# Kernel optimization log

Measured on AMD Instinct MI355X. Metric: run time of the kernel, lower is better.

Reference implementation:

```python
import jax, jax.numpy as jnp
import numpy as np
from jax import lax

B, T, F = 8, 512, 128          # batch, mel time, mel freq
DM, DS, DC, EXP, NL = 384, 16, 4, 2, 12
DI = EXP * DM                   # 768 inner width
DTR = (DM + 15) // 16           # 24, mamba_ssm dt_rank='auto'
PT = PF = 16
L = (T // PT) * (F // PF)       # 256 patches
NC = 4


def setup_inputs() -> dict:
    key = jax.random.key(0)
    ks = iter(jax.random.split(key, 24))
    def n(shape, s=0.02):
        return jax.random.normal(next(ks), shape, jnp.float32) * s
    return {
        "x": jax.random.normal(next(ks), (B, T, F), jnp.float32),
        "patch_w": n((DM, PT, PF)),
        "patch_b": jnp.zeros((DM,), jnp.float32),
        "pos_embed": n((1, L, DM)),
        "ln_g": jnp.ones((NL, DM), jnp.float32),
        "ln_b": jnp.zeros((NL, DM), jnp.float32),
        "in_proj_w": n((NL, 2 * DI, DM)),
        "conv_w": n((NL, DI, DC), 0.1),
        "conv_b": jnp.zeros((NL, DI), jnp.float32),
        "x_proj_w": n((NL, DTR + 2 * DS, DI)),
        "dt_proj_w": n((NL, DI, DTR), 0.1),
        "dt_proj_b": n((NL, DI), 0.1),
        "A_log": jnp.tile(jnp.log(jnp.arange(1, DS + 1, dtype=jnp.float32))[None, None, :], (NL, DI, 1)),
        "Dskip": jnp.ones((NL, DI), jnp.float32),
        "out_proj_w": n((NL, DM, DI)),
        "fn_g": jnp.ones((DM,), jnp.float32),
        "fn_b": jnp.zeros((DM,), jnp.float32),
        "head_w": n((NC, DM)),
        "head_b": jnp.zeros((NC,), jnp.float32),
    }


def _layernorm(x, g, b):
    m = x.mean(-1, keepdims=True)
    v = jnp.var(x, axis=-1, keepdims=True)
    return (x - m) * lax.rsqrt(v + 1e-5) * g + b


def _silu(v):
    return v * jax.nn.sigmoid(v)


def _mamba_block(x, p):
    # x: [B, L, DM]; residual Mamba block (pre-LN, dropout=identity in eval)
    ln_g, ln_b, Wi, cw, cb, Wx, Wdt, bdt, A_log, Dsk, Wo = p
    res = x
    h = _layernorm(x, ln_g, ln_b)
    xz = jnp.einsum('bld,ed->ble', h, Wi)          # [B,L,2*DI]
    u, z = jnp.split(xz, 2, axis=-1)
    # causal depthwise conv1d, kernel DC (small, unrolled)
    up = jnp.pad(u, ((0, 0), (DC - 1, 0), (0, 0)))
    u = sum(up[:, k:k + L, :] * cw[:, k] for k in range(DC)) + cb
    u = _silu(u)
    proj = jnp.einsum('bld,ed->ble', u, Wx)        # [B,L,DTR+2*DS]
    dt, Bm, Cm = jnp.split(proj, [DTR, DTR + DS], axis=-1)
    delta = jax.nn.softplus(jnp.einsum('blr,dr->bld', dt, Wdt) + bdt)  # [B,L,DI]
    A = -jnp.exp(A_log)                            # [DI, DS]
    dA = jnp.exp(delta[..., None] * A)             # [B,L,DI,DS]
    dBu = (delta * u)[..., None] * Bm[:, :, None, :]

    def step(hst, inp):
        dA_t, dBu_t, C_t = inp
        hst = dA_t * hst + dBu_t                   # [B,DI,DS]
        return hst, jnp.einsum('bdn,bn->bd', hst, C_t)

    h0 = jnp.zeros((x.shape[0], DI, DS), x.dtype)
    _, ys = lax.scan(step, h0, (dA.swapaxes(0, 1), dBu.swapaxes(0, 1), Cm.swapaxes(0, 1)))
    y = ys.swapaxes(0, 1) + u * Dsk                # [B,L,DI]
    y = y * _silu(z)
    return res + jnp.einsum('bld,ed->ble', y, Wo)


def reference(x, patch_w, patch_b, pos_embed, ln_g, ln_b, in_proj_w, conv_w, conv_b,
              x_proj_w, dt_proj_w, dt_proj_b, A_log, Dskip, out_proj_w,
              fn_g, fn_b, head_w, head_b):
    Bn = x.shape[0]
    # patch embed = non-overlapping 16x16 conv == blocked reshape + einsum
    patches = x.reshape(Bn, T // PT, PT, F // PF, PF)
    tok = jnp.einsum('bhpwq,dpq->bhwd', patches, patch_w) + patch_b
    tok = tok.reshape(Bn, L, DM) + pos_embed

    def layer(carry, p):
        return _mamba_block(carry, p), None

    tok, _ = lax.scan(layer, tok, (ln_g, ln_b, in_proj_w, conv_w, conv_b,
                                   x_proj_w, dt_proj_w, dt_proj_b, A_log, Dskip, out_proj_w))
    tok = _layernorm(tok, fn_g, fn_b)
    pooled = tok.mean(axis=1)
    return pooled @ head_w.T + head_b
```

## Files before the change

### kernel.cpp

```cpp
#include <hip/hip_runtime.h>
#include <math.h>

namespace {

constexpr int kB   = 8;
constexpr int kL   = 256;
constexpr int kTok = 2048;
constexpr int kDM  = 384;
constexpr int kDI  = 768;
constexpr int kDS  = 16;
constexpr int kDTR = 24;
constexpr int kPROJ = 56;
constexpr int kNL  = 12;

constexpr int kWIN  = 2 * kDI * kDM;
constexpr int kWOUT = kDM * kDI;
constexpr int kWX   = kPROJ * kDI;
constexpr int kWTOT = kWIN + kWOUT + kWX;

typedef float f32x4 __attribute__((ext_vector_type(4)));
typedef short short8 __attribute__((ext_vector_type(8)));

__device__ __forceinline__ float softplus_f(float x) {
  return (x > 20.f) ? x : log1pf(__expf(x));
}
__device__ __forceinline__ float silu_f(float x) {
  return x / (1.f + __expf(-x));
}
__device__ __forceinline__ unsigned short f2bf(float f) {
  union { float f; unsigned u; } v; v.f = f;
  unsigned r = v.u + 0x7FFFu + ((v.u >> 16) & 1u);
  return (unsigned short)(r >> 16);
}
__device__ __forceinline__ float bf2f(unsigned short u) {
  return __uint_as_float((unsigned)u << 16);
}

__global__ __launch_bounds__(256) void patch_gemm_k(
    const float* __restrict__ x, const float* __restrict__ Bw,
    const float* __restrict__ bias, const float* __restrict__ pos,
    float* __restrict__ C) {
  __shared__ float As[16][68];
  __shared__ float Bs[16][68];
  int tid = threadIdx.x;
  int bm = blockIdx.y * 64;
  int bn = blockIdx.x * 64;
  int lr = tid >> 2;
  int lk = (tid & 3) << 2;
  int tm = (tid >> 4) << 2;
  int tn = (tid & 15) << 2;
  float acc[4][4] = {};
  for (int k0 = 0; k0 < 256; k0 += 16) {
    {
      int token = bm + lr;
      int b = token >> 8, l = token & 255;
      int h = l >> 3, w = l & 7;
      int p = k0 >> 4;
      const float* ap = x + ((size_t)(b * 512) + h * 16 + p) * 128 + w * 16 + lk;
      float4 av = *(const float4*)ap;
      As[lk + 0][lr] = av.x; As[lk + 1][lr] = av.y;
      As[lk + 2][lr] = av.z; As[lk + 3][lr] = av.w;
    }
    {
      const float* bp = Bw + (size_t)(bn + lr) * 256 + k0 + lk;
      float4 bv = *(const float4*)bp;
      Bs[lk + 0][lr] = bv.x; Bs[lk + 1][lr] = bv.y;
      Bs[lk + 2][lr] = bv.z; Bs[lk + 3][lr] = bv.w;
    }
    __syncthreads();
    #pragma unroll
    for (int k = 0; k < 16; ++k) {
      float4 a = *(const float4*)&As[k][tm];
      float4 b = *(const float4*)&Bs[k][tn];
      float av[4] = {a.x, a.y, a.z, a.w};
      float bv[4] = {b.x, b.y, b.z, b.w};
      #pragma unroll
      for (int i = 0; i < 4; ++i)
        #pragma unroll
        for (int j = 0; j < 4; ++j)
          acc[i][j] = fmaf(av[i], bv[j], acc[i][j]);
    }
    __syncthreads();
  }
  #pragma unroll
  for (int i = 0; i < 4; ++i) {
    int row = bm + tm + i;
    #pragma unroll
    for (int j = 0; j < 4; ++j) {
      int col = bn + tn + j;
      C[(size_t)row * kDM + col] =
          acc[i][j] + bias[col] + pos[(size_t)(row & 255) * kDM + col];
    }
  }
}

__global__ __launch_bounds__(384) void lnpool_k(
    const float* __restrict__ in, float* __restrict__ pooled,
    const float* __restrict__ g, const float* __restrict__ bb) {
  int t = blockIdx.x, d = threadIdx.x;
  float v = in[(size_t)t * kDM + d];
  float s = v, s2 = v * v;
  #pragma unroll
  for (int m = 32; m >= 1; m >>= 1) {
    s  += __shfl_xor(s, m);
    s2 += __shfl_xor(s2, m);
  }
  __shared__ float ps[6], ps2[6];
  if ((d & 63) == 0) { ps[d >> 6] = s; ps2[d >> 6] = s2; }
  __syncthreads();
  float S = 0.f, S2 = 0.f;
  #pragma unroll
  for (int i = 0; i < 6; ++i) { S += ps[i]; S2 += ps2[i]; }
  float mean = S * (1.f / 384.f);
  float var  = S2 * (1.f / 384.f) - mean * mean;
  float r = rsqrtf(var + 1e-5f);
  float o = (v - mean) * r * g[d] + bb[d];
  atomicAdd(&pooled[(size_t)(t >> 8) * kDM + d], o * (1.f / 256.f));
}

__global__ __launch_bounds__(256) void convert_all_k(
    const float* __restrict__ w_in, const float* __restrict__ w_out,
    const float* __restrict__ w_x, unsigned short* __restrict__ dst,
    float* __restrict__ pooled_zero) {
  int layer = blockIdx.y;
  int tid = threadIdx.x;
  if (layer == 0 && blockIdx.x == 0) {
    for (int i = tid; i < kB * kDM; i += 256) pooled_zero[i] = 0.f;
  }
  int i4 = (blockIdx.x * 256 + tid) * 4;
  if (i4 >= kWTOT) return;
  const float* src;
  int off;
  if (i4 < kWIN) { src = w_in + (size_t)layer * kWIN; off = i4; }
  else if (i4 < kWIN + kWOUT) { src = w_out + (size_t)layer * kWOUT; off = i4 - kWIN; }
  else { src = w_x + (size_t)layer * kWX; off = i4 - kWIN - kWOUT; }
  float4 v = *(const float4*)(src + off);
  unsigned short o[4] = {f2bf(v.x), f2bf(v.y), f2bf(v.z), f2bf(v.w)};
  *(uint2*)(dst + (size_t)layer * kWTOT + i4) = *(const uint2*)o;
}

__global__ __launch_bounds__(256) void inproj_ln_k(
    const float* __restrict__ tok, const unsigned short* __restrict__ Bw,
    const float* __restrict__ g, const float* __restrict__ bb,
    unsigned short* __restrict__ Cbf, float* __restrict__ proj_zero) {
  __shared__ __align__(16) unsigned short As[4][64][8];
  __shared__ __align__(16) unsigned short Bs[4][128][8];
  __shared__ float smean[64], srstd[64];
  __shared__ float sg_[kDM], sb_[kDM];
  int tid = threadIdx.x;
  int bm = blockIdx.y * 64;
  int bn = blockIdx.x * 128;
  {
    int bid = blockIdx.y * 12 + blockIdx.x;
    for (int i = bid * 256 + tid; i < kTok * kPROJ; i += 384 * 256)
      proj_zero[i] = 0.f;
  }
  for (int i = tid; i < kDM; i += 256) { sg_[i] = g[i]; sb_[i] = bb[i]; }
  {
    int r = tid >> 2, quarter = tid & 3;
    const float* rp = tok + (size_t)(bm + r) * kDM + quarter * 96;
    float s = 0.f, s2 = 0.f;
    #pragma unroll
    for (int q = 0; q < 24; ++q) {
      float4 v = ((const float4*)rp)[q];
      s  += v.x + v.y + v.z + v.w;
      s2 += v.x * v.x + v.y * v.y + v.z * v.z + v.w * v.w;
    }
    s  += __shfl_xor(s, 1);  s2 += __shfl_xor(s2, 1);
    s  += __shfl_xor(s, 2);  s2 += __shfl_xor(s2, 2);
    if (quarter == 0) {
      float mean = s * (1.f / 384.f);
      float var  = s2 * (1.f / 384.f) - mean * mean;
      smean[r] = mean;
      srstd[r] = rsqrtf(var + 1e-5f);
    }
  }
  __syncthreads();
  int wave = tid >> 6, lane = tid & 63;
  int lm = lane & 15, lq = lane >> 4;
  int wm = (wave & 1) * 32, wn = (wave >> 1) * 64;
  f32x4 acc[2][4] = {};
  for (int k0 = 0; k0 < kDM; k0 += 32) {
    int ar = tid & 63, aq = tid >> 6;
    unsigned short av[8];
    {
      float mean = smean[ar], rstd = srstd[ar];
      const float* ap = tok + (size_t)(bm + ar) * kDM + k0 + aq * 8;
      float4 v0 = ((const float4*)ap)[0];
      float4 v1 = ((const float4*)ap)[1];
      float vv[8] = {v0.x, v0.y, v0.z, v0.w, v1.x, v1.y, v1.z, v1.w};
      #pragma unroll
      for (int j = 0; j < 8; ++j) {
        int k = k0 + aq * 8 + j;
        av[j] = f2bf((vv[j] - mean) * rstd * sg_[k] + sb_[k]);
      }
    }
    int br = tid & 127, bq0 = tid >> 7, bq1 = bq0 + 2;
    uint4 b0 = *(const uint4*)(Bw + (size_t)(bn + br) * kDM + k0 + bq0 * 8);
    uint4 b1 = *(const uint4*)(Bw + (size_t)(bn + br) * kDM + k0 + bq1 * 8);
    __syncthreads();
    *(uint4*)&As[aq][ar][0]  = *(const uint4*)av;
    *(uint4*)&Bs[bq0][br][0] = b0;
    *(uint4*)&Bs[bq1][br][0] = b1;
    __syncthreads();
    short8 bfrag[4];
    #pragma unroll
    for (int ni = 0; ni < 4; ++ni)
      bfrag[ni] = *(const short8*)&Bs[lq][wn + ni * 16 + lm][0];
    #pragma unroll
    for (int mi = 0; mi < 2; ++mi) {
      short8 afrag = *(const short8*)&As[lq][wm + mi * 16 + lm][0];
      #pragma unroll
      for (int ni = 0; ni < 4; ++ni)
        acc[mi][ni] = __builtin_amdgcn_mfma_f32_16x16x32_bf16(
            afrag, bfrag[ni], acc[mi][ni], 0, 0, 0);
    }
  }
  #pragma unroll
  for (int mi = 0; mi < 2; ++mi) {
    #pragma unroll
    for (int ni = 0; ni < 4; ++ni) {
      int grow0 = bm + wm + mi * 16 + lq * 4;
      int gcol = bn + wn + ni * 16 + lm;
      #pragma unroll
      for (int r = 0; r < 4; ++r)
        Cbf[(size_t)(grow0 + r) * (2 * kDI) + gcol] = f2bf(acc[mi][ni][r]);
    }
  }
}

__global__ __launch_bounds__(256) void xproj_conv_k(
    const unsigned short* __restrict__ xz, const unsigned short* __restrict__ Bw,
    const float* __restrict__ cw, const float* __restrict__ cb,
    float* __restrict__ proj, unsigned short* __restrict__ uT_bf,
    unsigned short* __restrict__ sgT_bf) {
  __shared__ __align__(16) unsigned short As[4][64][8];
  __shared__ __align__(16) unsigned short Bs[4][64][8];
  __shared__ float scw[128][4];
  __shared__ float scb[128];
  int tid = threadIdx.x;
  int bm = blockIdx.x * 64;
  int kbase = blockIdx.y * 128;
  int wave = tid >> 6, lane = tid & 63;
  int lm = lane & 15, lq = lane >> 4;
  int wm = wave * 16;
  f32x4 acc[4] = {};

  if (tid < 128) {
    *(float4*)&scw[tid][0] = *(const float4*)(cw + (size_t)(kbase + tid) * 4);
    scb[tid] = cb[kbase + tid];
  }
  __syncthreads();

  int ar = tid & 63;
  int aq = tid >> 6;
  int t = bm + ar;
  int b = t >> 8, l = t & 255;

  for (int kt = 0; kt < 4; ++kt) {
    int k0 = kbase + kt * 32;
    int dloc = kt * 32 + aq * 8;
    int dg = kbase + dloc;
    unsigned short av[8];
    {
      float vals[4][8];
      #pragma unroll
      for (int q = 0; q < 4; ++q) {
        if (l - 3 + q >= 0) {
          uint4 r = *(const uint4*)(xz + (size_t)(t - 3 + q) * (2 * kDI) + dg);
          const unsigned short* rs = (const unsigned short*)&r;
          #pragma unroll
          for (int j = 0; j < 8; ++j) vals[q][j] = bf2f(rs[j]);
        } else {
          #pragma unroll
          for (int j = 0; j < 8; ++j) vals[q][j] = 0.f;
        }
      }
      uint4 zr = *(const uint4*)(xz + (size_t)t * (2 * kDI) + kDI + dg);
      const unsigned short* zs = (const unsigned short*)&zr;
      #pragma unroll
      for (int j = 0; j < 8; ++j) {
        float a = scb[dloc + j];
        a = fmaf(vals[0][j], scw[dloc + j][0], a);
        a = fmaf(vals[1][j], scw[dloc + j][1], a);
        a = fmaf(vals[2][j], scw[dloc + j][2], a);
        a = fmaf(vals[3][j], scw[dloc + j][3], a);
        unsigned short ub = f2bf(silu_f(a));
        av[j] = ub;
        size_t rbase = ((size_t)b * kDI + dg + j) * kL + l;
        uT_bf[rbase] = ub;
        sgT_bf[rbase] = f2bf(silu_f(bf2f(zs[j])));
      }
    }
    int br = tid & 63, bq = tid >> 6;
    uint4 b0;
    if (br < kPROJ)
      b0 = *(const uint4*)(Bw + (size_t)br * kDI + k0 + bq * 8);
    else
      b0 = make_uint4(0u, 0u, 0u, 0u);
    __syncthreads();
    *(uint4*)&As[aq][ar][0] = *(const uint4*)av;
    *(uint4*)&Bs[bq][br][0] = b0;
    __syncthreads();
    short8 afrag = *(const short8*)&As[lq][wm + lm][0];
    #pragma unroll
    for (int ni = 0; ni < 4; ++ni) {
      short8 bfrag = *(const short8*)&Bs[lq][ni * 16 + lm][0];
      acc[ni] = __builtin_amdgcn_mfma_f32_16x16x32_bf16(
          afrag, bfrag, acc[ni], 0, 0, 0);
    }
  }

  #pragma unroll
  for (int ni = 0; ni < 4; ++ni) {
    int grow0 = bm + wm + lq * 4;
    int gcol = ni * 16 + lm;
    if (gcol < kPROJ) {
      #pragma unroll
      for (int r = 0; r < 4; ++r)
        atomicAdd(&proj[(size_t)(grow0 + r) * kPROJ + gcol], acc[ni][r]);
    }
  }
}

__global__ __launch_bounds__(256) void bgemm_out_k(
    const unsigned short* __restrict__ A, int lda,
    const unsigned short* __restrict__ B, int ldb,
    float* __restrict__ C, int ldc, int Kc) {
  __shared__ __align__(16) unsigned short As[4][128][8];
  __shared__ __align__(16) unsigned short Bs[4][128][8];
  int tid = threadIdx.x;
  int bm = blockIdx.y * 128;
  int bn = blockIdx.x * 128;
  int k_begin = blockIdx.z * Kc;
  int wave = tid >> 6, lane = tid & 63;
  int lm = lane & 15, lq = lane >> 4;
  int wm = (wave >> 1) * 64, wn = (wave & 1) * 64;
  f32x4 acc[4][4] = {};

  for (int kt = 0; kt < Kc; kt += 32) {
    int k0 = k_begin + kt;
    int ar0 = tid & 127, aq0 = tid >> 7;
    int aq1 = aq0 + 2;
    uint4 a0 = *(const uint4*)(A + (size_t)(bm + ar0) * lda + k0 + aq0 * 8);
    uint4 a1 = *(const uint4*)(A + (size_t)(bm + ar0) * lda + k0 + aq1 * 8);
    uint4 b0 = *(const uint4*)(B + (size_t)(bn + ar0) * ldb + k0 + aq0 * 8);
    uint4 b1 = *(const uint4*)(B + (size_t)(bn + ar0) * ldb + k0 + aq1 * 8);
    __syncthreads();
    *(uint4*)&As[aq0][ar0][0] = a0;
    *(uint4*)&As[aq1][ar0][0] = a1;
    *(uint4*)&Bs[aq0][ar0][0] = b0;
    *(uint4*)&Bs[aq1][ar0][0] = b1;
    __syncthreads();
    short8 bfrag[4];
    #pragma unroll
    for (int ni = 0; ni < 4; ++ni)
      bfrag[ni] = *(const short8*)&Bs[lq][wn + ni * 16 + lm][0];
    #pragma unroll
    for (int mi = 0; mi < 4; ++mi) {
      short8 afrag = *(const short8*)&As[lq][wm + mi * 16 + lm][0];
      #pragma unroll
      for (int ni = 0; ni < 4; ++ni)
        acc[mi][ni] = __builtin_amdgcn_mfma_f32_16x16x32_bf16(
            afrag, bfrag[ni], acc[mi][ni], 0, 0, 0);
    }
  }

  #pragma unroll
  for (int mi = 0; mi < 4; ++mi) {
    #pragma unroll
    for (int ni = 0; ni < 4; ++ni) {
      int grow0 = bm + wm + mi * 16 + lq * 4;
      int gcol = bn + wn + ni * 16 + lm;
      #pragma unroll
      for (int r = 0; r < 4; ++r)
        atomicAdd(&C[(size_t)(grow0 + r) * ldc + gcol], acc[mi][ni][r]);
    }
  }
}

__global__ __launch_bounds__(256, 5) void scansplit_k(
    const float* __restrict__ proj, const unsigned short* __restrict__ uT_bf,
    const unsigned short* __restrict__ sgT_bf, const float* __restrict__ dtw,
    const float* __restrict__ dtb, const float* __restrict__ A_log,
    const float* __restrict__ Dsk, unsigned short* __restrict__ y_bf) {
  int d0 = blockIdx.x * 4;
  int b = blockIdx.y;
  int tid = threadIdx.x;
  int dsub = tid & 3;
  int nq = (tid >> 2) & 3;
  int c = tid >> 4;
  int d = d0 + dsub;
  __shared__ float sdt[16][16][5];
  __shared__ float sh[16][16][5];
  __shared__ float sca[16][16][5];

  float Av2[4];
  {
    const float kLog2e = 1.44269504088896340736f;
    float4 v = *(const float4*)(A_log + (size_t)d * kDS + nq * 4);
    Av2[0] = -__expf(v.x) * kLog2e;
    Av2[1] = -__expf(v.y) * kLog2e;
    Av2[2] = -__expf(v.z) * kLog2e;
    Av2[3] = -__expf(v.w) * kLog2e;
  }
  float bdt = dtb[d];
  float Dv = Dsk[d];

  const float* pr = proj + ((size_t)(b * kL) + c * 16) * kPROJ;

  {
    float wdt[24];
    const float* wp = dtw + (size_t)d * kDTR;
    #pragma unroll
    for (int q = 0; q < 6; ++q) {
      float4 v = ((const float4*)wp)[q];
      wdt[q * 4 + 0] = v.x; wdt[q * 4 + 1] = v.y;
      wdt[q * 4 + 2] = v.z; wdt[q * 4 + 3] = v.w;
    }
    #pragma unroll
    for (int i = 0; i < 4; ++i) {
      const float* p = pr + (size_t)(nq * 4 + i) * kPROJ;
      float acc = bdt;
      #pragma unroll
      for (int q = 0; q < 6; ++q) {
        float4 v = ((const float4*)p)[q];
        acc = fmaf(v.x, wdt[q * 4 + 0], acc);
        acc = fmaf(v.y, wdt[q * 4 + 1], acc);
        acc = fmaf(v.z, wdt[q * 4 + 2], acc);
        acc = fmaf(v.w, wdt[q * 4 + 3], acc);
      }
      sdt[c][nq * 4 + i][dsub] = softplus_f(acc);
    }
  }

  union { uint4 v[2]; unsigned short s[16]; } uu;
  {
    const unsigned short* up = uT_bf + ((size_t)b * kDI + d) * kL + c * 16;
    uu.v[0] = ((const uint4*)up)[0];
    uu.v[1] = ((const uint4*)up)[1];
  }
  __syncthreads();

  float h[4] = {}, ca[4] = {1.f, 1.f, 1.f, 1.f};
  #pragma unroll
  for (int i = 0; i < 16; ++i) {
    float dl = sdt[c][i][dsub];
    float du = dl * bf2f(uu.s[i]);
    float4 Bq = *(const float4*)(pr + (size_t)i * kPROJ + 24 + nq * 4);
    float Bv[4] = {Bq.x, Bq.y, Bq.z, Bq.w};
    #pragma unroll
    for (int n = 0; n < 4; ++n) {
      float a = exp2f(dl * Av2[n]);
      h[n] = fmaf(a, h[n], du * Bv[n]);
      ca[n] *= a;
    }
  }
  {
    int nrow = nq * 4;
    #pragma unroll
    for (int n = 0; n < 4; ++n) {
      sh[c][nrow + n][dsub] = h[n];
      sca[c][nrow + n][dsub] = ca[n];
    }
  }
  __syncthreads();

  float h0[4] = {};
  {
    int nrow = nq * 4;
    for (int j = 0; j < c; ++j) {
      #pragma unroll
      for (int n = 0; n < 4; ++n)
        h0[n] = fmaf(sca[j][nrow + n][dsub], h0[n], sh[j][nrow + n][dsub]);
    }
  }

  union { uint4 v[2]; unsigned short s[16]; } zz;
  zz.v[0] = make_uint4(0u, 0u, 0u, 0u);
  zz.v[1] = make_uint4(0u, 0u, 0u, 0u);
  if (nq == 0) {
    const unsigned short* sp = sgT_bf + ((size_t)b * kDI + d) * kL + c * 16;
    zz.v[0] = ((const uint4*)sp)[0];
    zz.v[1] = ((const uint4*)sp)[1];
  }

  unsigned short* yp = y_bf + (size_t)(b * kL + c * 16) * kDI + d;
  #pragma unroll
  for (int i = 0; i < 16; ++i) {
    float dl = sdt[c][i][dsub];
    float uv = bf2f(uu.s[i]);
    float du = dl * uv;
    const float* p = pr + (size_t)i * kPROJ + 24 + nq * 4;
    float4 Bq = *(const float4*)p;
    float4 Cq = *(const float4*)(p + 16);
    float Bv[4] = {Bq.x, Bq.y, Bq.z, Bq.w};
    float Cv[4] = {Cq.x, Cq.y, Cq.z, Cq.w};
    float yv = 0.f;
    #pragma unroll
    for (int n = 0; n < 4; ++n) {
      float a = exp2f(dl * Av2[n]);
      h0[n] = fmaf(a, h0[n], du * Bv[n]);
      yv = fmaf(h0[n], Cv[n], yv);
    }
    yv += __shfl_xor(yv, 4);
    yv += __shfl_xor(yv, 8);
    if (nq == 0) yp[(size_t)i * kDI] = f2bf((yv + uv * Dv) * bf2f(zz.s[i]));
  }
}

__global__ __launch_bounds__(64) void head_k(
    const float* __restrict__ pooled, const float* __restrict__ hw,
    const float* __restrict__ hb, float* __restrict__ out) {
  int b = blockIdx.x >> 2, c = blockIdx.x & 3;
  int lane = threadIdx.x;
  float acc = 0.f;
  for (int dd = lane; dd < kDM; dd += 64)
    acc = fmaf(pooled[b * kDM + dd], hw[c * kDM + dd], acc);
  #pragma unroll
  for (int m = 32; m >= 1; m >>= 1) acc += __shfl_xor(acc, m);
  if (lane == 0) out[b * 4 + c] = acc + hb[c];
}

}

extern "C" void kernel_launch(void* const* d_in, const int* in_sizes, int n_in,
                              void* d_out, int out_size, void* d_ws, size_t ws_size,
                              hipStream_t stream) {
  (void)in_sizes; (void)n_in; (void)out_size; (void)ws_size;
  const float* x        = (const float*)d_in[0];
  const float* patch_w  = (const float*)d_in[1];
  const float* patch_b  = (const float*)d_in[2];
  const float* pos      = (const float*)d_in[3];
  const float* ln_g     = (const float*)d_in[4];
  const float* ln_b     = (const float*)d_in[5];
  const float* in_w     = (const float*)d_in[6];
  const float* conv_w   = (const float*)d_in[7];
  const float* conv_b   = (const float*)d_in[8];
  const float* xproj_w  = (const float*)d_in[9];
  const float* dtproj_w = (const float*)d_in[10];
  const float* dtproj_b = (const float*)d_in[11];
  const float* A_log    = (const float*)d_in[12];
  const float* Dskip    = (const float*)d_in[13];
  const float* out_w    = (const float*)d_in[14];
  const float* fn_g     = (const float*)d_in[15];
  const float* fn_b     = (const float*)d_in[16];
  const float* head_w   = (const float*)d_in[17];
  const float* head_b   = (const float*)d_in[18];
  float* out = (float*)d_out;

  float* ws = (float*)d_ws;
  float* tok    = ws; ws += kTok * kDM;
  float* proj   = ws; ws += kTok * kPROJ;
  float* pooled = ws; ws += kB * kDM;
  unsigned short* xz_bf  = (unsigned short*)ws; ws += kTok * 2 * kDI / 2;
  unsigned short* uT_bf  = (unsigned short*)ws; ws += kTok * kDI / 2;
  unsigned short* sgT_bf = (unsigned short*)ws; ws += kTok * kDI / 2;
  unsigned short* y_bf   = (unsigned short*)ws; ws += kTok * kDI / 2;
  unsigned short* w_bf   = (unsigned short*)ws; ws += (size_t)kNL * kWTOT / 2;

  convert_all_k<<<dim3(kWTOT / 4 / 256, kNL), 256, 0, stream>>>(
      in_w, out_w, xproj_w, w_bf, pooled);

  patch_gemm_k<<<dim3(6, 32), 256, 0, stream>>>(x, patch_w, patch_b, pos, tok);

  for (int layer = 0; layer < kNL; ++layer) {
    const unsigned short* wl = w_bf + (size_t)layer * kWTOT;
    inproj_ln_k<<<dim3(12, 32), 256, 0, stream>>>(
        tok, wl, ln_g + layer * kDM, ln_b + layer * kDM, xz_bf, proj);
    xproj_conv_k<<<dim3(32, 6), 256, 0, stream>>>(
        xz_bf, wl + kWIN + kWOUT, conv_w + layer * kDI * 4,
        conv_b + layer * kDI, proj, uT_bf, sgT_bf);
    scansplit_k<<<dim3(kDI / 4, kB), 256, 0, stream>>>(
        proj, uT_bf, sgT_bf, dtproj_w + (size_t)layer * kDI * kDTR,
        dtproj_b + layer * kDI, A_log + (size_t)layer * kDI * kDS,
        Dskip + layer * kDI, y_bf);
    bgemm_out_k<<<dim3(3, 16, 4), 256, 0, stream>>>(
        y_bf, kDI, wl + kWIN, kDI, tok, kDM, kDI / 4);
  }

  lnpool_k<<<kTok, kDM, 0, stream>>>(tok, pooled, fn_g, fn_b);
  head_k<<<kB * 4, 64, 0, stream>>>(pooled, head_w, head_b, out);
}
```

Baseline: 1.133 ms.

## Stage proj rows in LDS for scan and shrink out-proj GEMM tiles

The selective-scan kernel now loads each batch's proj rows into a shared-memory tile once, first the dt columns and then the B/C columns. The dt projection, B and C are then read from LDS rather than repeatedly from global memory. The chunk decay product is computed as exp2 of the summed delta instead of a running product, and the occupancy hint drops from 5 to 3 to make room for the larger shared footprint. Separately, the output-projection GEMM goes from 128x128 to 64x64 tiles with four times as many blocks, trading per-block reuse for more parallelism.

```diff
diff --git a/kernel.cpp b/kernel.cpp
--- a/kernel.cpp
+++ b/kernel.cpp
@@ -327,49 +327,44 @@
     const unsigned short* __restrict__ A, int lda,
     const unsigned short* __restrict__ B, int ldb,
     float* __restrict__ C, int ldc, int Kc) {
-  __shared__ __align__(16) unsigned short As[4][128][8];
-  __shared__ __align__(16) unsigned short Bs[4][128][8];
+  __shared__ __align__(16) unsigned short As[4][64][8];
+  __shared__ __align__(16) unsigned short Bs[4][64][8];
   int tid = threadIdx.x;
-  int bm = blockIdx.y * 128;
-  int bn = blockIdx.x * 128;
+  int bm = blockIdx.y * 64;
+  int bn = blockIdx.x * 64;
   int k_begin = blockIdx.z * Kc;
   int wave = tid >> 6, lane = tid & 63;
   int lm = lane & 15, lq = lane >> 4;
-  int wm = (wave >> 1) * 64, wn = (wave & 1) * 64;
-  f32x4 acc[4][4] = {};
+  int wm = (wave & 1) * 32, wn = (wave >> 1) * 32;
+  f32x4 acc[2][2] = {};
 
   for (int kt = 0; kt < Kc; kt += 32) {
     int k0 = k_begin + kt;
-    int ar0 = tid & 127, aq0 = tid >> 7;
-    int aq1 = aq0 + 2;
-    uint4 a0 = *(const uint4*)(A + (size_t)(bm + ar0) * lda + k0 + aq0 * 8);
-    uint4 a1 = *(const uint4*)(A + (size_t)(bm + ar0) * lda + k0 + aq1 * 8);
-    uint4 b0 = *(const uint4*)(B + (size_t)(bn + ar0) * ldb + k0 + aq0 * 8);
-    uint4 b1 = *(const uint4*)(B + (size_t)(bn + ar0) * ldb + k0 + aq1 * 8);
-    __syncthreads();
-    *(uint4*)&As[aq0][ar0][0] = a0;
-    *(uint4*)&As[aq1][ar0][0] = a1;
-    *(uint4*)&Bs[aq0][ar0][0] = b0;
-    *(uint4*)&Bs[aq1][ar0][0] = b1;
-    __syncthreads();
-    short8 bfrag[4];
-    #pragma unroll
-    for (int ni = 0; ni < 4; ++ni)
+    int ar = tid & 63, aq = tid >> 6;
+    uint4 a0 = *(const uint4*)(A + (size_t)(bm + ar) * lda + k0 + aq * 8);
+    uint4 b0 = *(const uint4*)(B + (size_t)(bn + ar) * ldb + k0 + aq * 8);
+    __syncthreads();
+    *(uint4*)&As[aq][ar][0] = a0;
+    *(uint4*)&Bs[aq][ar][0] = b0;
+    __syncthreads();
+    short8 bfrag[2];
+    #pragma unroll
+    for (int ni = 0; ni < 2; ++ni)
       bfrag[ni] = *(const short8*)&Bs[lq][wn + ni * 16 + lm][0];
     #pragma unroll
-    for (int mi = 0; mi < 4; ++mi) {
+    for (int mi = 0; mi < 2; ++mi) {
       short8 afrag = *(const short8*)&As[lq][wm + mi * 16 + lm][0];
       #pragma unroll
-      for (int ni = 0; ni < 4; ++ni)
+      for (int ni = 0; ni < 2; ++ni)
         acc[mi][ni] = __builtin_amdgcn_mfma_f32_16x16x32_bf16(
             afrag, bfrag[ni], acc[mi][ni], 0, 0, 0);
     }
   }
 
   #pragma unroll
-  for (int mi = 0; mi < 4; ++mi) {
-    #pragma unroll
-    for (int ni = 0; ni < 4; ++ni) {
+  for (int mi = 0; mi < 2; ++mi) {
+    #pragma unroll
+    for (int ni = 0; ni < 2; ++ni) {
       int grow0 = bm + wm + mi * 16 + lq * 4;
       int gcol = bn + wn + ni * 16 + lm;
       #pragma unroll
@@ -379,7 +374,7 @@
   }
 }
 
-__global__ __launch_bounds__(256, 5) void scansplit_k(
+__global__ __launch_bounds__(256, 3) void scansplit_k(
     const float* __restrict__ proj, const unsigned short* __restrict__ uT_bf,
     const unsigned short* __restrict__ sgT_bf, const float* __restrict__ dtw,
     const float* __restrict__ dtb, const float* __restrict__ A_log,
@@ -391,9 +386,24 @@
   int nq = (tid >> 2) & 3;
   int c = tid >> 4;
   int d = d0 + dsub;
+  __shared__ float sproj[256][33];
   __shared__ float sdt[16][16][5];
   __shared__ float sh[16][16][5];
   __shared__ float sca[16][16][5];
+
+  const float* pr0 = proj + (size_t)(b * kL) * kPROJ;
+
+  {
+    const float* rp = pr0 + (size_t)tid * kPROJ;
+    #pragma unroll
+    for (int q = 0; q < 6; ++q) {
+      float4 v = ((const float4*)rp)[q];
+      sproj[tid][q * 4 + 0] = v.x;
+      sproj[tid][q * 4 + 1] = v.y;
+      sproj[tid][q * 4 + 2] = v.z;
+      sproj[tid][q * 4 + 3] = v.w;
+    }
+  }
 
   float Av2[4];
   {
@@ -407,10 +417,8 @@
   float bdt = dtb[d];
   float Dv = Dsk[d];
 
-  const float* pr = proj + ((size_t)(b * kL) + c * 16) * kPROJ;
-
-  {
-    float wdt[24];
+  float wdt[24];
+  {
     const float* wp = dtw + (size_t)d * kDTR;
     #pragma unroll
     for (int q = 0; q < 6; ++q) {
@@ -418,20 +426,6 @@
       wdt[q * 4 + 0] = v.x; wdt[q * 4 + 1] = v.y;
       wdt[q * 4 + 2] = v.z; wdt[q * 4 + 3] = v.w;
     }
-    #pragma unroll
-    for (int i = 0; i < 4; ++i) {
-      const float* p = pr + (size_t)(nq * 4 + i) * kPROJ;
-      float acc = bdt;
-      #pragma unroll
-      for (int q = 0; q < 6; ++q) {
-        float4 v = ((const float4*)p)[q];
-        acc = fmaf(v.x, wdt[q * 4 + 0], acc);
-        acc = fmaf(v.y, wdt[q * 4 + 1], acc);
-        acc = fmaf(v.z, wdt[q * 4 + 2], acc);
-        acc = fmaf(v.w, wdt[q * 4 + 3], acc);
-      }
-      sdt[c][nq * 4 + i][dsub] = softplus_f(acc);
-    }
   }
 
   union { uint4 v[2]; unsigned short s[16]; } uu;
@@ -440,20 +434,44 @@
     uu.v[0] = ((const uint4*)up)[0];
     uu.v[1] = ((const uint4*)up)[1];
   }
-  __syncthreads();
-
-  float h[4] = {}, ca[4] = {1.f, 1.f, 1.f, 1.f};
+
+  __syncthreads();
+
+  #pragma unroll
+  for (int i = 0; i < 4; ++i) {
+    int tok = c * 16 + nq * 4 + i;
+    float acc = bdt;
+    #pragma unroll
+    for (int r = 0; r < 24; ++r) acc = fmaf(sproj[tok][r], wdt[r], acc);
+    sdt[c][nq * 4 + i][dsub] = softplus_f(acc);
+  }
+  __syncthreads();
+
+  {
+    const float* rp = pr0 + (size_t)tid * kPROJ + 24;
+    #pragma unroll
+    for (int q = 0; q < 8; ++q) {
+      float4 v = ((const float4*)rp)[q];
+      sproj[tid][q * 4 + 0] = v.x;
+      sproj[tid][q * 4 + 1] = v.y;
+      sproj[tid][q * 4 + 2] = v.z;
+      sproj[tid][q * 4 + 3] = v.w;
+    }
+  }
+  __syncthreads();
+
+  float h[4] = {};
+  float S = 0.f;
   #pragma unroll
   for (int i = 0; i < 16; ++i) {
+    int tok = c * 16 + i;
     float dl = sdt[c][i][dsub];
     float du = dl * bf2f(uu.s[i]);
-    float4 Bq = *(const float4*)(pr + (size_t)i * kPROJ + 24 + nq * 4);
-    float Bv[4] = {Bq.x, Bq.y, Bq.z, Bq.w};
+    S += dl;
     #pragma unroll
     for (int n = 0; n < 4; ++n) {
       float a = exp2f(dl * Av2[n]);
-      h[n] = fmaf(a, h[n], du * Bv[n]);
-      ca[n] *= a;
+      h[n] = fmaf(a, h[n], du * sproj[tok][nq * 4 + n]);
     }
   }
   {
@@ -461,7 +479,7 @@
     #pragma unroll
     for (int n = 0; n < 4; ++n) {
       sh[c][nrow + n][dsub] = h[n];
-      sca[c][nrow + n][dsub] = ca[n];
+      sca[c][nrow + n][dsub] = exp2f(S * Av2[n]);
     }
   }
   __syncthreads();
@@ -488,20 +506,16 @@
   unsigned short* yp = y_bf + (size_t)(b * kL + c * 16) * kDI + d;
   #pragma unroll
   for (int i = 0; i < 16; ++i) {
+    int tok = c * 16 + i;
     float dl = sdt[c][i][dsub];
     float uv = bf2f(uu.s[i]);
     float du = dl * uv;
-    const float* p = pr + (size_t)i * kPROJ + 24 + nq * 4;
-    float4 Bq = *(const float4*)p;
-    float4 Cq = *(const float4*)(p + 16);
-    float Bv[4] = {Bq.x, Bq.y, Bq.z, Bq.w};
-    float Cv[4] = {Cq.x, Cq.y, Cq.z, Cq.w};
     float yv = 0.f;
     #pragma unroll
     for (int n = 0; n < 4; ++n) {
       float a = exp2f(dl * Av2[n]);
-      h0[n] = fmaf(a, h0[n], du * Bv[n]);
-      yv = fmaf(h0[n], Cv[n], yv);
+      h0[n] = fmaf(a, h0[n], du * sproj[tok][nq * 4 + n]);
+      yv = fmaf(h0[n], sproj[tok][16 + nq * 4 + n], yv);
     }
     yv += __shfl_xor(yv, 4);
     yv += __shfl_xor(yv, 8);
@@ -575,7 +589,7 @@
         proj, uT_bf, sgT_bf, dtproj_w + (size_t)layer * kDI * kDTR,
         dtproj_b + layer * kDI, A_log + (size_t)layer * kDI * kDS,
         Dskip + layer * kDI, y_bf);
-    bgemm_out_k<<<dim3(3, 16, 4), 256, 0, stream>>>(
+    bgemm_out_k<<<dim3(6, 32, 4), 256, 0, stream>>>(
         y_bf, kDI, wl + kWIN, kDI, tok, kDM, kDI / 4);
   }
 
```

Result: slower. 1.164 ms (+2.7%).

## Transpose x_proj output and stage it in shared memory for scan kernel

Applied to the files above, without the earlier changes.

The x_proj atomic accumulation now writes a token-contiguous transposed buffer. The scan kernel stages the per-batch dt, B and C rows into shared memory with coalesced loads instead of strided per-thread float4 reads from global memory. It also replaces the running product of decay factors with a single exp2 of the summed delta. The large shared array lowers the occupancy hint from 5 to 3 blocks, and the transposed atomics are more scattered in the x_proj kernel.

```diff
diff --git a/kernel.cpp b/kernel.cpp
--- a/kernel.cpp
+++ b/kernel.cpp
@@ -232,7 +232,7 @@
 __global__ __launch_bounds__(256) void xproj_conv_k(
     const unsigned short* __restrict__ xz, const unsigned short* __restrict__ Bw,
     const float* __restrict__ cw, const float* __restrict__ cb,
-    float* __restrict__ proj, unsigned short* __restrict__ uT_bf,
+    float* __restrict__ projT, unsigned short* __restrict__ uT_bf,
     unsigned short* __restrict__ sgT_bf) {
   __shared__ __align__(16) unsigned short As[4][64][8];
   __shared__ __align__(16) unsigned short Bs[4][64][8];
@@ -318,7 +318,7 @@
     if (gcol < kPROJ) {
       #pragma unroll
       for (int r = 0; r < 4; ++r)
-        atomicAdd(&proj[(size_t)(grow0 + r) * kPROJ + gcol], acc[ni][r]);
+        atomicAdd(&projT[(size_t)gcol * kTok + grow0 + r], acc[ni][r]);
     }
   }
 }
@@ -379,8 +379,8 @@
   }
 }
 
-__global__ __launch_bounds__(256, 5) void scansplit_k(
-    const float* __restrict__ proj, const unsigned short* __restrict__ uT_bf,
+__global__ __launch_bounds__(256, 3) void scansplit_k(
+    const float* __restrict__ projT, const unsigned short* __restrict__ uT_bf,
     const unsigned short* __restrict__ sgT_bf, const float* __restrict__ dtw,
     const float* __restrict__ dtb, const float* __restrict__ A_log,
     const float* __restrict__ Dsk, unsigned short* __restrict__ y_bf) {
@@ -391,9 +391,16 @@
   int nq = (tid >> 2) & 3;
   int c = tid >> 4;
   int d = d0 + dsub;
+  __shared__ float sp[32][257];
   __shared__ float sdt[16][16][5];
   __shared__ float sh[16][16][5];
   __shared__ float sca[16][16][5];
+
+  const float* pT = projT + (size_t)b * kL;
+
+  #pragma unroll
+  for (int r = 0; r < 24; ++r)
+    sp[r][tid] = pT[(size_t)r * kTok + tid];
 
   float Av2[4];
   {
@@ -407,10 +414,8 @@
   float bdt = dtb[d];
   float Dv = Dsk[d];
 
-  const float* pr = proj + ((size_t)(b * kL) + c * 16) * kPROJ;
-
-  {
-    float wdt[24];
+  float wdt[24];
+  {
     const float* wp = dtw + (size_t)d * kDTR;
     #pragma unroll
     for (int q = 0; q < 6; ++q) {
@@ -418,20 +423,6 @@
       wdt[q * 4 + 0] = v.x; wdt[q * 4 + 1] = v.y;
       wdt[q * 4 + 2] = v.z; wdt[q * 4 + 3] = v.w;
     }
-    #pragma unroll
-    for (int i = 0; i < 4; ++i) {
-      const float* p = pr + (size_t)(nq * 4 + i) * kPROJ;
-      float acc = bdt;
-      #pragma unroll
-      for (int q = 0; q < 6; ++q) {
-        float4 v = ((const float4*)p)[q];
-        acc = fmaf(v.x, wdt[q * 4 + 0], acc);
-        acc = fmaf(v.y, wdt[q * 4 + 1], acc);
-        acc = fmaf(v.z, wdt[q * 4 + 2], acc);
-        acc = fmaf(v.w, wdt[q * 4 + 3], acc);
-      }
-      sdt[c][nq * 4 + i][dsub] = softplus_f(acc);
-    }
   }
 
   union { uint4 v[2]; unsigned short s[16]; } uu;
@@ -440,20 +431,36 @@
     uu.v[0] = ((const uint4*)up)[0];
     uu.v[1] = ((const uint4*)up)[1];
   }
-  __syncthreads();
-
-  float h[4] = {}, ca[4] = {1.f, 1.f, 1.f, 1.f};
+
+  __syncthreads();
+
+  #pragma unroll
+  for (int i = 0; i < 4; ++i) {
+    int tk = c * 16 + nq * 4 + i;
+    float acc = bdt;
+    #pragma unroll
+    for (int r = 0; r < 24; ++r) acc = fmaf(sp[r][tk], wdt[r], acc);
+    sdt[c][nq * 4 + i][dsub] = softplus_f(acc);
+  }
+  __syncthreads();
+
+  #pragma unroll
+  for (int r = 0; r < 32; ++r)
+    sp[r][tid] = pT[(size_t)(24 + r) * kTok + tid];
+  __syncthreads();
+
+  float h[4] = {};
+  float S = 0.f;
   #pragma unroll
   for (int i = 0; i < 16; ++i) {
+    int tk = c * 16 + i;
     float dl = sdt[c][i][dsub];
     float du = dl * bf2f(uu.s[i]);
-    float4 Bq = *(const float4*)(pr + (size_t)i * kPROJ + 24 + nq * 4);
-    float Bv[4] = {Bq.x, Bq.y, Bq.z, Bq.w};
+    S += dl;
     #pragma unroll
     for (int n = 0; n < 4; ++n) {
       float a = exp2f(dl * Av2[n]);
-      h[n] = fmaf(a, h[n], du * Bv[n]);
-      ca[n] *= a;
+      h[n] = fmaf(a, h[n], du * sp[nq * 4 + n][tk]);
     }
   }
   {
@@ -461,7 +468,7 @@
     #pragma unroll
     for (int n = 0; n < 4; ++n) {
       sh[c][nrow + n][dsub] = h[n];
-      sca[c][nrow + n][dsub] = ca[n];
+      sca[c][nrow + n][dsub] = exp2f(S * Av2[n]);
     }
   }
   __syncthreads();
@@ -480,28 +487,24 @@
   zz.v[0] = make_uint4(0u, 0u, 0u, 0u);
   zz.v[1] = make_uint4(0u, 0u, 0u, 0u);
   if (nq == 0) {
-    const unsigned short* sp = sgT_bf + ((size_t)b * kDI + d) * kL + c * 16;
-    zz.v[0] = ((const uint4*)sp)[0];
-    zz.v[1] = ((const uint4*)sp)[1];
+    const unsigned short* sp2 = sgT_bf + ((size_t)b * kDI + d) * kL + c * 16;
+    zz.v[0] = ((const uint4*)sp2)[0];
+    zz.v[1] = ((const uint4*)sp2)[1];
   }
 
   unsigned short* yp = y_bf + (size_t)(b * kL + c * 16) * kDI + d;
   #pragma unroll
   for (int i = 0; i < 16; ++i) {
+    int tk = c * 16 + i;
     float dl = sdt[c][i][dsub];
     float uv = bf2f(uu.s[i]);
     float du = dl * uv;
-    const float* p = pr + (size_t)i * kPROJ + 24 + nq * 4;
-    float4 Bq = *(const float4*)p;
-    float4 Cq = *(const float4*)(p + 16);
-    float Bv[4] = {Bq.x, Bq.y, Bq.z, Bq.w};
-    float Cv[4] = {Cq.x, Cq.y, Cq.z, Cq.w};
     float yv = 0.f;
     #pragma unroll
     for (int n = 0; n < 4; ++n) {
       float a = exp2f(dl * Av2[n]);
-      h0[n] = fmaf(a, h0[n], du * Bv[n]);
-      yv = fmaf(h0[n], Cv[n], yv);
+      h0[n] = fmaf(a, h0[n], du * sp[nq * 4 + n][tk]);
+      yv = fmaf(h0[n], sp[16 + nq * 4 + n][tk], yv);
     }
     yv += __shfl_xor(yv, 4);
     yv += __shfl_xor(yv, 8);
@@ -551,7 +554,7 @@
 
   float* ws = (float*)d_ws;
   float* tok    = ws; ws += kTok * kDM;
-  float* proj   = ws; ws += kTok * kPROJ;
+  float* projT  = ws; ws += kTok * kPROJ;
   float* pooled = ws; ws += kB * kDM;
   unsigned short* xz_bf  = (unsigned short*)ws; ws += kTok * 2 * kDI / 2;
   unsigned short* uT_bf  = (unsigned short*)ws; ws += kTok * kDI / 2;
@@ -567,12 +570,12 @@
   for (int layer = 0; layer < kNL; ++layer) {
     const unsigned short* wl = w_bf + (size_t)layer * kWTOT;
     inproj_ln_k<<<dim3(12, 32), 256, 0, stream>>>(
-        tok, wl, ln_g + layer * kDM, ln_b + layer * kDM, xz_bf, proj);
+        tok, wl, ln_g + layer * kDM, ln_b + layer * kDM, xz_bf, projT);
     xproj_conv_k<<<dim3(32, 6), 256, 0, stream>>>(
         xz_bf, wl + kWIN + kWOUT, conv_w + layer * kDI * 4,
-        conv_b + layer * kDI, proj, uT_bf, sgT_bf);
+        conv_b + layer * kDI, projT, uT_bf, sgT_bf);
     scansplit_k<<<dim3(kDI / 4, kB), 256, 0, stream>>>(
-        proj, uT_bf, sgT_bf, dtproj_w + (size_t)layer * kDI * kDTR,
+        projT, uT_bf, sgT_bf, dtproj_w + (size_t)layer * kDI * kDTR,
         dtproj_b + layer * kDI, A_log + (size_t)layer * kDI * kDS,
         Dskip + layer * kDI, y_bf);
     bgemm_out_k<<<dim3(3, 16, 4), 256, 0, stream>>>(
```

New measurement: 1.248 ms. 1.1x slower.
